# Kernel tuning notes

Hardware: AMD Instinct MI355X
Metric: run time of the kernel (lower is better)

## Reference

```python
import jax, jax.numpy as jnp
import numpy as np

EPS = 1e-6
N_HEADS, N_KV = 16, 4


def rmsnorm(x, w):
    return x * jax.lax.rsqrt(jnp.mean(x * x, axis=-1, keepdims=True) + EPS) * w


def setup_inputs() -> dict:
    key = jax.random.key(0)
    ks = jax.random.split(key, 9)
    B, T, D, F = 2, 2048, 2048, 8192
    KVD = N_KV * (D // N_HEADS)
    s = lambda k, shape, fan: (jax.random.normal(k, shape, jnp.float32) * (fan ** -0.5))
    return {
        "x": jax.random.normal(ks[0], (B, T, D), jnp.float32),
        "norm1_w": jnp.ones((D,), jnp.float32),
        "norm2_w": jnp.ones((D,), jnp.float32),
        "Wq": s(ks[1], (D, D), D),
        "Wk": s(ks[2], (D, KVD), D),
        "Wv": s(ks[3], (D, KVD), D),
        "Wo": s(ks[4], (D, D), D),
        "Wc": s(ks[5], (D, D), D),
        "W1": s(ks[6], (D, F), D),
        "W2": s(ks[7], (F, D), F),
        "W3": s(ks[8], (D, F), D),
    }


def reference(x, norm1_w, norm2_w, Wq, Wk, Wv, Wo, Wc, W1, W2, W3):
    B, T, D = x.shape
    dh = D // N_HEADS          # 128
    G = N_HEADS // N_KV        # groups per kv head
    scale = dh ** -0.5

    xn = rmsnorm(x, norm1_w)
    q = xn @ Wq                               # [B,T,D]
    pos = q @ Wc                              # CoPE stand-in: contextual positional bias on Q
    q = (q + pos).reshape(B, T, N_KV, G, dh)  # group q heads under their kv head
    k = (xn @ Wk).reshape(B, T, N_KV, dh)
    v = (xn @ Wv).reshape(B, T, N_KV, dh)

    # GQA without repeat_interleave: contract each group against shared K/V
    scores = jnp.einsum('bqkgd,bskd->bkgqs', q, k) * scale   # [B,KV,G,T,T]
    i = jnp.arange(T)
    causal = i[:, None] >= i[None, :]
    scores = jnp.where(causal, scores, -jnp.inf)
    w = jax.nn.softmax(scores, axis=-1)
    att = jnp.einsum('bkgqs,bskd->bqkgd', w, v).reshape(B, T, D)

    x = x + att @ Wo
    xn2 = rmsnorm(x, norm2_w)
    x = x + (jax.nn.silu(xn2 @ W1) * (xn2 @ W3)) @ W2
    return x
```

## Files before the change

### kernel.cpp

```cpp
#include <hip/hip_runtime.h>
#include <hip/hip_bf16.h>

typedef __attribute__((ext_vector_type(8))) short short8;
typedef __attribute__((ext_vector_type(4))) float floatx4;
typedef unsigned short ushort_t;

__device__ inline float b2f(ushort_t s) {
    return __uint_as_float(((unsigned int)s) << 16);
}
__device__ inline ushort_t f2b(float f) {
    unsigned int u = __float_as_uint(f);
    unsigned int r = 0x7fff + ((u >> 16) & 1);
    return (ushort_t)((u + r) >> 16);
}
__device__ inline unsigned int cvtpk(float lo, float hi) {
    unsigned int r;
    asm("v_cvt_pk_bf16_f32 %0, %1, %2" : "=v"(r) : "v"(lo), "v"(hi));
    return r;
}
__device__ inline void load8(const float* p, float* f) {
    float4 a = *(const float4*)p;
    float4 b = *(const float4*)(p + 4);
    f[0] = a.x; f[1] = a.y; f[2] = a.z; f[3] = a.w;
    f[4] = b.x; f[5] = b.y; f[6] = b.z; f[7] = b.w;
}
__device__ inline void gload16(const ushort_t* g, ushort_t* l) {
    __builtin_amdgcn_global_load_lds(
        (const __attribute__((address_space(1))) unsigned int*)g,
        (__attribute__((address_space(3))) unsigned int*)l, 16, 0, 0);
}
__device__ inline void lbar() {
    asm volatile("s_waitcnt lgkmcnt(0)" ::: "memory");
    __builtin_amdgcn_s_barrier();
    asm volatile("" ::: "memory");
}

__global__ __launch_bounds__(256) void transpose_all(
    const float* __restrict__ s0, const float* __restrict__ s1,
    const float* __restrict__ s2, const float* __restrict__ s3,
    const float* __restrict__ s4, const float* __restrict__ s5,
    const float* __restrict__ s6, const float* __restrict__ s7,
    ushort_t* d0, ushort_t* d1, ushort_t* d2, ushort_t* d3,
    ushort_t* d4, ushort_t* d5, ushort_t* d6, ushort_t* d7) {
    int id = blockIdx.x;
    const float* src; ushort_t* dst; int K, N;
    if (id < 1024)       { src = s0; dst = d0; K = 2048; N = 2048; }
    else if (id < 1280)  { id -= 1024;  src = s1; dst = d1; K = 2048; N = 512; }
    else if (id < 1536)  { id -= 1280;  src = s2; dst = d2; K = 2048; N = 512; }
    else if (id < 2560)  { id -= 1536;  src = s3; dst = d3; K = 2048; N = 2048; }
    else if (id < 3584)  { id -= 2560;  src = s4; dst = d4; K = 2048; N = 2048; }
    else if (id < 7680)  { id -= 3584;  src = s5; dst = d5; K = 2048; N = 8192; }
    else if (id < 11776) { id -= 7680;  src = s6; dst = d6; K = 2048; N = 8192; }
    else                 { id -= 11776; src = s7; dst = d7; K = 8192; N = 2048; }
    int tn = N >> 6;
    int kb = (id / tn) * 64, nb = (id % tn) * 64;
    __shared__ ushort_t tile[64][65];
    int t = threadIdx.x;
#pragma unroll
    for (int i = 0; i < 4; ++i) {
        int r = (t >> 4) + i * 16;
        int c = (t & 15) * 4;
        float4 v = *(const float4*)(src + (size_t)(kb + r) * N + nb + c);
        tile[c + 0][r] = f2b(v.x);
        tile[c + 1][r] = f2b(v.y);
        tile[c + 2][r] = f2b(v.z);
        tile[c + 3][r] = f2b(v.w);
    }
    __syncthreads();
#pragma unroll
    for (int i = 0; i < 2; ++i) {
        int s = t + i * 256;
        int n = s >> 3, kc = (s & 7) * 8;
        ushort_t o[8];
#pragma unroll
        for (int j = 0; j < 8; ++j) o[j] = tile[n][kc + j];
        *(uint4*)(dst + (size_t)(nb + n) * K + kb + kc) = *(const uint4*)o;
    }
}

__global__ __launch_bounds__(256) void rmsnorm_kernel(const float* __restrict__ x,
                                                      const float* __restrict__ w,
                                                      ushort_t* __restrict__ out, int D) {
    int row = blockIdx.x;
    int t = threadIdx.x;
    const float* xr = x + (size_t)row * D;
    float f[8];
    load8(xr + t * 8, f);
    float ss = 0.f;
#pragma unroll
    for (int i = 0; i < 8; ++i) ss += f[i] * f[i];
#pragma unroll
    for (int m = 1; m < 64; m <<= 1) ss += __shfl_xor(ss, m);
    __shared__ float wsum[4];
    if ((t & 63) == 0) wsum[t >> 6] = ss;
    __syncthreads();
    float tot = wsum[0] + wsum[1] + wsum[2] + wsum[3];
    float r = rsqrtf(tot / (float)D + 1e-6f);
    float wf[8];
    load8(w + t * 8, wf);
    ushort_t o[8];
#pragma unroll
    for (int i = 0; i < 8; ++i) o[i] = f2b(f[i] * r * wf[i]);
    *(uint4*)(out + (size_t)row * D + t * 8) = *(const uint4*)o;
}

__global__ __launch_bounds__(256) void reduce_out(const ushort_t* __restrict__ p,
                                                  const float* __restrict__ resid,
                                                  float* __restrict__ out, int n) {
    int stride = gridDim.x * 256;
    for (int i = blockIdx.x * 256 + threadIdx.x; i * 8 < n; i += stride) {
        int i8 = i * 8;
        uint4 a = *(const uint4*)(p + i8);
        uint4 b = *(const uint4*)(p + n + i8);
        const ushort_t* ae = (const ushort_t*)&a;
        const ushort_t* be = (const ushort_t*)&b;
        float rr[8];
        load8(resid + i8, rr);
        float o[8];
#pragma unroll
        for (int j = 0; j < 8; ++j) o[j] = b2f(ae[j]) + b2f(be[j]) + rr[j];
        *(float4*)(out + i8) = make_float4(o[0], o[1], o[2], o[3]);
        *(float4*)(out + i8 + 4) = make_float4(o[4], o[5], o[6], o[7]);
    }
}

__device__ inline void vm6() { asm volatile("s_waitcnt vmcnt(6)" ::: "memory"); }
__device__ inline void vm4() { asm volatile("s_waitcnt vmcnt(4)" ::: "memory"); }

template <int MODE>
__global__ __launch_bounds__(512, 2) void gemm8(const ushort_t* __restrict__ A,
                                                const ushort_t* __restrict__ Bt,
                                                const ushort_t* __restrict__ aux,
                                                const float* __restrict__ aux2,
                                                void* __restrict__ Cv,
                                                void* __restrict__ C2v,
                                                void* __restrict__ C3v,
                                                int M, int N, int Ksub, int lda) {
    __shared__ __align__(16) ushort_t Lds[2 * 32768];
    const int tid = threadIdx.x;
    const int wv = tid >> 6, lane = tid & 63;
    const int l16 = lane & 15, l4 = lane >> 4;
    const int wr = wv >> 2, wc = wv & 3;
    int nwg = gridDim.x;
    int per = nwg >> 3;
    int wg = (blockIdx.x & 7) * per + (blockIdx.x >> 3);
    int mtiles = M >> 8;
    int bx = wg & (mtiles - 1);
    int by = wg / mtiles;
    int bm = bx << 8, bn = by << 8;
    int koff = blockIdx.y * Ksub;

    const int sr = tid >> 3;
    const int scol = (((tid & 7) ^ (sr & 7)) << 3);
    const ushort_t* gA = A + (size_t)(bm + sr) * lda + scol + koff;
    const ushort_t* gB = Bt + (size_t)(bn + sr) * lda + scol + koff;
    ushort_t* ldsw = Lds + wv * 512;

    const int ktiles = Ksub >> 6;
    const int niter = ktiles >> 1;
    const int km = ktiles - 1;

#define STG_A(slot, j, kt) gload16(gA + (size_t)((j) * 64) * lda + ((kt) << 6), ldsw + (slot) * 32768 + (j) * 4096)
#define STG_B(slot, j, kt) gload16(gB + (size_t)((j) * 64) * lda + ((kt) << 6), ldsw + (slot) * 32768 + 16384 + (j) * 4096)

    STG_A(0, 0, 0); STG_A(0, 2, 0); STG_A(0, 1, 0); STG_A(0, 3, 0);
    STG_B(0, 0, 0); STG_B(0, 1, 0); STG_B(0, 2, 0); STG_B(0, 3, 0);
    STG_A(1, 0, 1); STG_A(1, 2, 1);
    STG_B(1, 0, 1); STG_B(1, 1, 1); STG_B(1, 2, 1); STG_B(1, 3, 1);
    vm6();
    asm volatile("" ::: "memory");
    __builtin_amdgcn_s_barrier();

    const int lx = l4 ^ (l16 & 7);
    floatx4 acc[8][4] = {};
    short8 aR[4][2], bR[4][2];

#define DSA(slot, mh) { _Pragma("unroll") for (int m = 0; m < 4; ++m) { \
    _Pragma("unroll") for (int kk = 0; kk < 2; ++kk) \
      aR[m][kk] = *(const short8*)(Lds + (slot) * 32768 + \
          (wr * 128 + (mh) * 64 + m * 16 + l16) * 64 + ((lx ^ (kk << 2)) << 3)); } }
#define DSB(slot, nh) { _Pragma("unroll") for (int n = 0; n < 2; ++n) { \
    _Pragma("unroll") for (int kk = 0; kk < 2; ++kk) \
      bR[(nh) * 2 + n][kk] = *(const short8*)(Lds + (slot) * 32768 + 16384 + \
          (wc * 64 + ((nh) * 2 + n) * 16 + l16) * 64 + ((lx ^ (kk << 2)) << 3)); } }
#define QUAD(mh, nlo) { _Pragma("unroll") for (int m = 0; m < 4; ++m) \
    _Pragma("unroll") for (int n = 0; n < 2; ++n) \
    _Pragma("unroll") for (int kk = 0; kk < 2; ++kk) \
      acc[(mh) * 4 + m][(nlo) + n] = __builtin_amdgcn_mfma_f32_16x16x32_bf16( \
          aR[m][kk], bR[(nlo) + n][kk], acc[(mh) * 4 + m][(nlo) + n], 0, 0, 0); }
#define PHASE(DS, ST, MH, NLO, VM) { \
    DS; ST; \
    asm volatile("" ::: "memory"); \
    __builtin_amdgcn_s_barrier(); \
    asm volatile("s_waitcnt lgkmcnt(0)" ::: "memory"); \
    __builtin_amdgcn_sched_barrier(0); \
    __builtin_amdgcn_s_setprio(1); \
    QUAD(MH, NLO); \
    __builtin_amdgcn_s_setprio(0); \
    VM; \
    asm volatile("" ::: "memory"); \
    __builtin_amdgcn_s_barrier(); }

    for (int it = 0; it < niter; ++it) {
        int t1 = 2 * it + 1;
        int t2 = (2 * it + 2) & km;
        int t3 = (2 * it + 3) & km;
        PHASE({ DSA(0, 0); DSB(0, 0); }, { STG_A(1, 1, t1); STG_A(1, 3, t1); }, 0, 0, );
        PHASE({ DSB(0, 1); },            { STG_A(0, 0, t2); STG_A(0, 2, t2); }, 0, 2, );
        PHASE({ DSA(0, 1); },            { STG_B(0, 0, t2); STG_B(0, 1, t2); }, 1, 2, );
        PHASE({ },                       { STG_B(0, 2, t2); STG_B(0, 3, t2); }, 1, 0, vm6(); );
        PHASE({ DSA(1, 0); DSB(1, 0); }, { STG_A(0, 1, t2); STG_A(0, 3, t2); }, 0, 0, );
        PHASE({ DSB(1, 1); },            { STG_A(1, 0, t3); STG_A(1, 2, t3); }, 0, 2, );
        PHASE({ DSA(1, 1); },            { STG_B(1, 0, t3); STG_B(1, 1, t3); }, 1, 2, );
        PHASE({ },                       { STG_B(1, 2, t3); STG_B(1, 3, t3); }, 1, 0, vm6(); );
    }

#pragma unroll
    for (int mi = 0; mi < 8; ++mi)
#pragma unroll
        for (int ni = 0; ni < 4; ++ni)
#pragma unroll
            for (int r = 0; r < 4; ++r) {
                int row = bm + wr * 128 + mi * 16 + l4 * 4 + r;
                int col = bn + wc * 64 + ni * 16 + l16;
                size_t idx = (size_t)row * N + col;
                float v = acc[mi][ni][r];
                if (MODE == 0) {
                    ((ushort_t*)Cv)[idx] = f2b(v);
                } else if (MODE == 1) {
                    ((ushort_t*)Cv)[idx] = f2b(v + b2f(aux[idx]));
                } else if (MODE == 2) {
                    float h = b2f(aux[idx]);
                    ((ushort_t*)Cv)[idx] = f2b((h / (1.f + __expf(-h))) * v);
                } else if (MODE == 3) {
                    ((ushort_t*)Cv)[(size_t)blockIdx.y * M * N + idx] = f2b(v);
                } else if (MODE == 5) {
                    ((float*)Cv)[idx] = v + aux2[idx];
                } else if (MODE == 6) {
                    if (bn < 2048) {
                        ((ushort_t*)Cv)[(size_t)row * 2048 + col] = f2b(v);
                    } else if (bn < 2560) {
                        ((ushort_t*)C2v)[(size_t)row * 512 + (col - 2048)] = f2b(v);
                    } else {
                        ((ushort_t*)C3v)[(size_t)(col - 2560) * 4096 + row] = f2b(v);
                    }
                }
            }
#undef STG_A
#undef STG_B
#undef DSA
#undef DSB
#undef QUAD
#undef PHASE
}

template <int MODE>
__global__ __launch_bounds__(512, 1) void gemm8h(const ushort_t* __restrict__ A,
                                                 const ushort_t* __restrict__ Bt,
                                                 const ushort_t* __restrict__ aux,
                                                 const float* __restrict__ aux2,
                                                 void* __restrict__ Cv,
                                                 int M, int N, int K) {
    __shared__ __align__(16) ushort_t Lds[2 * 24576];
    const int tid = threadIdx.x;
    const int wv = tid >> 6, lane = tid & 63;
    const int l16 = lane & 15, l4 = lane >> 4;
    const int wr = wv >> 2, wc = wv & 3;
    int nwg = gridDim.x;
    int per = nwg >> 3;
    int wg = (blockIdx.x & 7) * per + (blockIdx.x >> 3);
    int mtiles = M >> 7;
    int bx = wg & (mtiles - 1);
    int by = wg / mtiles;
    int bm = bx << 7, bn = by << 8;

    const int sr = tid >> 3;
    const int scol = (((tid & 7) ^ (sr & 7)) << 3);
    const ushort_t* gA = A + (size_t)(bm + sr) * K + scol;
    const ushort_t* gB = Bt + (size_t)(bn + sr) * K + scol;
    ushort_t* ldsw = Lds + wv * 512;

    const int ktiles = K >> 6;
    const int niter = ktiles >> 1;
    const int km = ktiles - 1;

#define HSTG_A(slot, j, kt) gload16(gA + (size_t)((j) * 64) * K + ((kt) << 6), ldsw + (slot) * 24576 + (j) * 4096)
#define HSTG_B(slot, j, kt) gload16(gB + (size_t)((j) * 64) * K + ((kt) << 6), ldsw + (slot) * 24576 + 8192 + (j) * 4096)

    HSTG_A(0, 0, 0); HSTG_A(0, 1, 0);
    HSTG_B(0, 0, 0); HSTG_B(0, 1, 0); HSTG_B(0, 2, 0); HSTG_B(0, 3, 0);
    HSTG_A(1, 0, 1); HSTG_A(1, 1, 1);
    HSTG_B(1, 0, 1); HSTG_B(1, 1, 1);
    vm4();
    asm volatile("" ::: "memory");
    __builtin_amdgcn_s_barrier();

    const int lx = l4 ^ (l16 & 7);
    floatx4 acc[4][4] = {};
    short8 aR[2][2], bR[4][2];

#define HDSA(slot, mh) { _Pragma("unroll") for (int m = 0; m < 2; ++m) { \
    _Pragma("unroll") for (int kk = 0; kk < 2; ++kk) \
      aR[m][kk] = *(const short8*)(Lds + (slot) * 24576 + \
          (wr * 64 + (mh) * 32 + m * 16 + l16) * 64 + ((lx ^ (kk << 2)) << 3)); } }
#define HDSB(slot, nh) { _Pragma("unroll") for (int n = 0; n < 2; ++n) { \
    _Pragma("unroll") for (int kk = 0; kk < 2; ++kk) \
      bR[(nh) * 2 + n][kk] = *(const short8*)(Lds + (slot) * 24576 + 8192 + \
          (wc * 64 + ((nh) * 2 + n) * 16 + l16) * 64 + ((lx ^ (kk << 2)) << 3)); } }
#define HQUAD(mh, nlo) { _Pragma("unroll") for (int m = 0; m < 2; ++m) \
    _Pragma("unroll") for (int n = 0; n < 2; ++n) \
    _Pragma("unroll") for (int kk = 0; kk < 2; ++kk) \
      acc[(mh) * 2 + m][(nlo) + n] = __builtin_amdgcn_mfma_f32_16x16x32_bf16( \
          aR[m][kk], bR[(nlo) + n][kk], acc[(mh) * 2 + m][(nlo) + n], 0, 0, 0); }
#define HPHASE(DS, ST, MH, NLO, VM) { \
    DS; ST; \
    asm volatile("" ::: "memory"); \
    __builtin_amdgcn_s_barrier(); \
    asm volatile("s_waitcnt lgkmcnt(0)" ::: "memory"); \
    __builtin_amdgcn_sched_barrier(0); \
    __builtin_amdgcn_s_setprio(1); \
    HQUAD(MH, NLO); \
    __builtin_amdgcn_s_setprio(0); \
    VM; \
    asm volatile("" ::: "memory"); \
    __builtin_amdgcn_s_barrier(); }

    for (int it = 0; it < niter; ++it) {
        int t1 = 2 * it + 1;
        int t2 = (2 * it + 2) & km;
        int t3 = (2 * it + 3) & km;
        HPHASE({ HDSA(0, 0); HDSB(0, 0); }, { HSTG_B(1, 2, t1); HSTG_B(1, 3, t1); }, 0, 0, );
        HPHASE({ HDSB(0, 1); },             { },                                     0, 2, );
        HPHASE({ HDSA(0, 1); },             { HSTG_B(0, 0, t2); HSTG_B(0, 1, t2); }, 1, 2, );
        HPHASE({ },                         { HSTG_B(0, 2, t2); HSTG_B(0, 3, t2); }, 1, 0, vm4(); );
        HPHASE({ HDSA(1, 0); HDSB(1, 0); }, { HSTG_A(0, 0, t2); HSTG_A(0, 1, t2); }, 0, 0, );
        HPHASE({ HDSB(1, 1); },             { },                                     0, 2, );
        HPHASE({ HDSA(1, 1); },             { HSTG_B(1, 0, t3); HSTG_B(1, 1, t3); }, 1, 2, );
        HPHASE({ },                         { HSTG_A(1, 0, t3); HSTG_A(1, 1, t3); }, 1, 0, vm4(); );
    }

#pragma unroll
    for (int mi = 0; mi < 4; ++mi)
#pragma unroll
        for (int ni = 0; ni < 4; ++ni)
#pragma unroll
            for (int r = 0; r < 4; ++r) {
                int row = bm + wr * 64 + mi * 16 + l4 * 4 + r;
                int col = bn + wc * 64 + ni * 16 + l16;
                size_t idx = (size_t)row * N + col;
                float v = acc[mi][ni][r];
                if (MODE == 1) ((ushort_t*)Cv)[idx] = f2b(v + b2f(aux[idx]));
                else if (MODE == 5) ((float*)Cv)[idx] = v + aux2[idx];
            }
#undef HSTG_A
#undef HSTG_B
#undef HDSA
#undef HDSB
#undef HQUAD
#undef HPHASE
}

#define QB 64
#define SB 64

__global__ __launch_bounds__(256, 2) void attn_kernel(const ushort_t* __restrict__ Q,
                                                      const ushort_t* __restrict__ Kb,
                                                      const ushort_t* __restrict__ VbT,
                                                      ushort_t* __restrict__ O, int Tlen) {
    const int D = 2048, KVD = 512, dh = 128;
    const int MTOK = 4096;
    int p = blockIdx.x, h = blockIdx.y, b = blockIdx.z;
    int kv = h >> 2;
    int t = threadIdx.x, wave = t >> 6, lane = t & 63;
    int l16 = lane & 15, l4 = lane >> 4;
    __shared__ __align__(16) ushort_t Ks[2][SB][dh + 8];
    __shared__ __align__(16) ushort_t Vt[2][dh][SB + 8];
    __shared__ __align__(16) unsigned int Ps2[4][16][36];
    const float scale = 0.08838834764831845f;
    const ushort_t* Kg = Kb + ((size_t)(b * Tlen) + (t >> 4)) * KVD + kv * dh + (t & 15) * 8;
    const ushort_t* Vg = VbT + (size_t)(kv * dh + (t >> 3)) * MTOK + b * Tlen + (t & 7) * 8;

    for (int side = 0; side < 2; ++side) {
        int qt = side ? p : (31 - p);
        int qbase = qt * QB;
        int qfrag = qbase + wave * 16;
        int qcol = qfrag + l16;
        short8 qf[4];
        const ushort_t* Qrow = Q + ((size_t)(b * Tlen) + qfrag + l16) * D + h * dh;
#pragma unroll
        for (int kk = 0; kk < 4; ++kk) qf[kk] = *(const short8*)(Qrow + kk * 32 + l4 * 8);
        floatx4 o_acc[8] = {};
        float m_s = -INFINITY, l_s = 0.f;
        int nst = qt + 1;
        uint4 kreg[4], vreg[4];
#pragma unroll
        for (int p4 = 0; p4 < 4; ++p4) {
            kreg[p4] = *(const uint4*)(Kg + (size_t)(p4 * 16) * KVD);
            vreg[p4] = *(const uint4*)(Vg + (size_t)(p4 * 32) * MTOK);
        }
        lbar();
#pragma unroll
        for (int p4 = 0; p4 < 4; ++p4) {
            *(uint4*)(&Ks[0][(t >> 4) + p4 * 16][(t & 15) * 8]) = kreg[p4];
            *(uint4*)(&Vt[0][(t >> 3) + p4 * 32][(t & 7) * 8]) = vreg[p4];
        }
        if (nst > 1) {
#pragma unroll
            for (int p4 = 0; p4 < 4; ++p4) {
                kreg[p4] = *(const uint4*)(Kg + (size_t)(SB + p4 * 16) * KVD);
                vreg[p4] = *(const uint4*)(Vg + (size_t)(p4 * 32) * MTOK + SB);
            }
        }
        lbar();
        for (int st = 0; st < nst; ++st) {
            int cur = st & 1;
            int s0 = st * SB;
            if (st + 1 < nst) {
#pragma unroll
                for (int p4 = 0; p4 < 4; ++p4) {
                    *(uint4*)(&Ks[cur ^ 1][(t >> 4) + p4 * 16][(t & 15) * 8]) = kreg[p4];
                    *(uint4*)(&Vt[cur ^ 1][(t >> 3) + p4 * 32][(t & 7) * 8]) = vreg[p4];
                }
            }
            if (st + 2 < nst) {
                size_t off = (size_t)(st + 2) * SB;
#pragma unroll
                for (int p4 = 0; p4 < 4; ++p4) {
                    kreg[p4] = *(const uint4*)(Kg + (off + p4 * 16) * KVD);
                    vreg[p4] = *(const uint4*)(Vg + (size_t)(p4 * 32) * MTOK + off);
                }
            }
            floatx4 sa[4] = {};
            __builtin_amdgcn_s_setprio(1);
#pragma unroll
            for (int ss = 0; ss < 4; ++ss)
#pragma unroll
                for (int kk = 0; kk < 4; ++kk) {
                    short8 kf = *(const short8*)(&Ks[cur][ss * 16 + l16][kk * 32 + l4 * 8]);
                    sa[ss] = __builtin_amdgcn_mfma_f32_16x16x32_bf16(kf, qf[kk], sa[ss], 0, 0, 0);
                }
            __builtin_amdgcn_s_setprio(0);
            float sv[4][4];
            float pmax = -INFINITY;
#pragma unroll
            for (int ss = 0; ss < 4; ++ss)
#pragma unroll
                for (int r = 0; r < 4; ++r) {
                    int krow = s0 + ss * 16 + l4 * 4 + r;
                    float v = sa[ss][r] * scale;
                    if (krow > qcol) v = -INFINITY;
                    sv[ss][r] = v;
                    pmax = fmaxf(pmax, v);
                }
            pmax = fmaxf(pmax, __shfl_xor(pmax, 16));
            pmax = fmaxf(pmax, __shfl_xor(pmax, 32));
            bool skip = __all(pmax <= m_s + 8.f);
            float mn = skip ? m_s : fmaxf(m_s, pmax);
            float rsum = 0.f;
#pragma unroll
            for (int ss = 0; ss < 4; ++ss)
#pragma unroll
                for (int r = 0; r < 4; ++r) {
                    float pv = __expf(sv[ss][r] - mn);
                    sv[ss][r] = pv;
                    rsum += pv;
                }
            rsum += __shfl_xor(rsum, 16);
            rsum += __shfl_xor(rsum, 32);
            if (skip) {
                l_s += rsum;
            } else {
                float esc = __expf(m_s - mn);
                l_s = l_s * esc + rsum;
                m_s = mn;
                float ef[4];
#pragma unroll
                for (int r = 0; r < 4; ++r) ef[r] = __shfl(esc, l4 * 4 + r);
#pragma unroll
                for (int c = 0; c < 8; ++c)
#pragma unroll
                    for (int r = 0; r < 4; ++r) o_acc[c][r] *= ef[r];
            }
#pragma unroll
            for (int ss = 0; ss < 4; ++ss) {
                uint2 pk;
                pk.x = cvtpk(sv[ss][0], sv[ss][1]);
                pk.y = cvtpk(sv[ss][2], sv[ss][3]);
                *(uint2*)&Ps2[wave][l16][ss * 8 + l4 * 2] = pk;
            }
            short8 pa[2];
#pragma unroll
            for (int kk = 0; kk < 2; ++kk) {
                uint4 pv4 = *(const uint4*)&Ps2[wave][l16][kk * 16 + l4 * 4];
                pa[kk] = *(const short8*)&pv4;
            }
            __builtin_amdgcn_s_setprio(1);
#pragma unroll
            for (int c = 0; c < 8; ++c)
#pragma unroll
                for (int kk = 0; kk < 2; ++kk) {
                    short8 vf = *(const short8*)(&Vt[cur][c * 16 + l16][kk * 32 + l4 * 8]);
                    o_acc[c] = __builtin_amdgcn_mfma_f32_16x16x32_bf16(pa[kk], vf, o_acc[c], 0, 0, 0);
                }
            __builtin_amdgcn_s_setprio(0);
            lbar();
        }
        float linv[4];
#pragma unroll
        for (int r = 0; r < 4; ++r) linv[r] = 1.f / __shfl(l_s, l4 * 4 + r);
        ushort_t* Osh = &Ks[0][0][0];
#pragma unroll
        for (int c = 0; c < 8; ++c)
#pragma unroll
            for (int r = 0; r < 4; ++r)
                Osh[(wave * 16 + l4 * 4 + r) * 136 + c * 16 + l16] = f2b(o_acc[c][r] * linv[r]);
        lbar();
        {
            int orow = t >> 2, occ = (t & 3) * 32;
            const ushort_t* srcp = Osh + orow * 136 + occ;
            ushort_t* dstp = O + ((size_t)(b * Tlen) + qbase + orow) * D + h * dh + occ;
#pragma unroll
            for (int k = 0; k < 4; ++k)
                *(uint4*)(dstp + k * 8) = *(const uint4*)(srcp + k * 8);
        }
    }
}

extern "C" void kernel_launch(void* const* d_in, const int* in_sizes, int n_in,
                              void* d_out, int out_size, void* d_ws, size_t ws_size,
                              hipStream_t stream) {
    const float* x   = (const float*)d_in[0];
    const float* n1w = (const float*)d_in[1];
    const float* n2w = (const float*)d_in[2];
    const float* Wq  = (const float*)d_in[3];
    const float* Wk  = (const float*)d_in[4];
    const float* Wv  = (const float*)d_in[5];
    const float* Wo  = (const float*)d_in[6];
    const float* Wc  = (const float*)d_in[7];
    const float* W1  = (const float*)d_in[8];
    const float* W2  = (const float*)d_in[9];
    const float* W3  = (const float*)d_in[10];
    float* out = (float*)d_out;

    const int B = 2, T = 2048, D = 2048, F = 8192, KVD = 512;
    const int M = B * T;
    const size_t XD   = (size_t)M * D * 2;
    const size_t XDF  = (size_t)M * D * 4;
    const size_t KVSZ = (size_t)M * KVD * 2;
    const size_t MF   = (size_t)M * F * 2;
    const size_t WDD  = (size_t)D * D * 2;
    const size_t WQKV = (size_t)(D + 2 * KVD) * D * 2;
    const size_t WDF  = (size_t)D * F * 2;

    char* w = (char*)d_ws;
    ushort_t* xn    = (ushort_t*)(w);
    ushort_t* qtmp  = (ushort_t*)(w + XD);
    ushort_t* qfin  = (ushort_t*)(w + 2 * XD);
    float*    x2f   = (float*)   (w + 3 * XD);
    ushort_t* kbuf  = (ushort_t*)(w + 3 * XD + XDF);
    ushort_t* vbufT = (ushort_t*)(w + 3 * XD + XDF + KVSZ);
    ushort_t* h1    = (ushort_t*)(w + 3 * XD + XDF + 2 * KVSZ);
    char* wt = w + 3 * XD + XDF + 2 * KVSZ + MF;
    ushort_t* WqkvT = (ushort_t*)(wt);
    ushort_t* WcT   = (ushort_t*)(wt + WQKV);
    ushort_t* WoT   = (ushort_t*)(wt + WQKV + WDD);
    ushort_t* W1T   = (ushort_t*)(wt + WQKV + 2 * WDD);
    ushort_t* W3T   = (ushort_t*)(wt + WQKV + 2 * WDD + WDF);
    ushort_t* W2T   = (ushort_t*)(wt + WQKV + 2 * WDD + 2 * WDF);

    dim3 blk(256);
    dim3 blk8(512);

    transpose_all<<<15872, blk, 0, stream>>>(
        Wq, Wk, Wv, Wc, Wo, W1, W3, W2,
        WqkvT, WqkvT + (size_t)2048 * D, WqkvT + (size_t)2560 * D,
        WcT, WoT, W1T, W3T, W2T);

    rmsnorm_kernel<<<M, blk, 0, stream>>>(x, n1w, xn, D);
    gemm8<6><<<dim3((M / 256) * (3072 / 256)), blk8, 0, stream>>>(
        xn, WqkvT, nullptr, nullptr, qtmp, kbuf, vbufT, M, 3072, D, D);
    gemm8h<1><<<dim3((M / 128) * (D / 256)), blk8, 0, stream>>>(
        qtmp, WcT, qtmp, nullptr, qfin, M, D, D);
    attn_kernel<<<dim3(16, 16, B), blk, 0, stream>>>(qfin, kbuf, vbufT, qtmp, T);
    gemm8h<5><<<dim3((M / 128) * (D / 256)), blk8, 0, stream>>>(
        qtmp, WoT, nullptr, x, x2f, M, D, D);
    rmsnorm_kernel<<<M, blk, 0, stream>>>(x2f, n2w, xn, D);
    gemm8<0><<<dim3((M / 256) * (F / 256)), blk8, 0, stream>>>(
        xn, W1T, nullptr, nullptr, h1, nullptr, nullptr, M, F, D, D);
    gemm8<2><<<dim3((M / 256) * (F / 256)), blk8, 0, stream>>>(
        xn, W3T, h1, nullptr, h1, nullptr, nullptr, M, F, D, D);
    gemm8<3><<<dim3((M / 256) * (D / 256), 2), blk8, 0, stream>>>(
        h1, W2T, nullptr, nullptr, xn, nullptr, nullptr, M, D, F / 2, F);
    reduce_out<<<1024, blk, 0, stream>>>(xn, x2f, out, M * D);
}
```

Before: 791.6 us.

## Enlarge attention query tile to 128 rows with two fragments per wave

Each wave of the attention kernel now processes two 16-row query fragments (query block 128 instead of 64), so every K/V tile staged in shared memory feeds twice as many MFMAs. This halves K/V global loads and LDS staging per query and amortizes barriers. In exchange the grid halves to 256 blocks, occupancy drops to one block per CU via launch bounds, register pressure roughly doubles for accumulators, and causal masking wastes more work on the diagonal tile.

```diff
diff --git a/kernel.cpp b/kernel.cpp
--- a/kernel.cpp
+++ b/kernel.cpp
@@ -360,10 +360,10 @@
 #undef HPHASE
 }
 
-#define QB 64
+#define QB 128
 #define SB 64
 
-__global__ __launch_bounds__(256, 2) void attn_kernel(const ushort_t* __restrict__ Q,
+__global__ __launch_bounds__(256, 1) void attn_kernel(const ushort_t* __restrict__ Q,
                                                       const ushort_t* __restrict__ Kb,
                                                       const ushort_t* __restrict__ VbT,
                                                       ushort_t* __restrict__ O, int Tlen) {
@@ -375,23 +375,27 @@
     int l16 = lane & 15, l4 = lane >> 4;
     __shared__ __align__(16) ushort_t Ks[2][SB][dh + 8];
     __shared__ __align__(16) ushort_t Vt[2][dh][SB + 8];
-    __shared__ __align__(16) unsigned int Ps2[4][16][36];
+    __shared__ __align__(16) unsigned int Ps2[8][16][36];
     const float scale = 0.08838834764831845f;
     const ushort_t* Kg = Kb + ((size_t)(b * Tlen) + (t >> 4)) * KVD + kv * dh + (t & 15) * 8;
     const ushort_t* Vg = VbT + (size_t)(kv * dh + (t >> 3)) * MTOK + b * Tlen + (t & 7) * 8;
 
     for (int side = 0; side < 2; ++side) {
-        int qt = side ? p : (31 - p);
+        int qt = side ? p : (15 - p);
         int qbase = qt * QB;
-        int qfrag = qbase + wave * 16;
-        int qcol = qfrag + l16;
-        short8 qf[4];
-        const ushort_t* Qrow = Q + ((size_t)(b * Tlen) + qfrag + l16) * D + h * dh;
-#pragma unroll
-        for (int kk = 0; kk < 4; ++kk) qf[kk] = *(const short8*)(Qrow + kk * 32 + l4 * 8);
-        floatx4 o_acc[8] = {};
-        float m_s = -INFINITY, l_s = 0.f;
-        int nst = qt + 1;
+        int qw = qbase + wave * 32;
+        short8 qf[2][4];
+#pragma unroll
+        for (int f = 0; f < 2; ++f) {
+            const ushort_t* Qrow = Q + ((size_t)(b * Tlen) + qw + f * 16 + l16) * D + h * dh;
+#pragma unroll
+            for (int kk = 0; kk < 4; ++kk) qf[f][kk] = *(const short8*)(Qrow + kk * 32 + l4 * 8);
+        }
+        floatx4 o_acc[2][8] = {};
+        float m_s[2], l_s[2];
+#pragma unroll
+        for (int f = 0; f < 2; ++f) { m_s[f] = -INFINITY; l_s[f] = 0.f; }
+        int nst = 2 * qt + 2;
         uint4 kreg[4], vreg[4];
 #pragma unroll
         for (int p4 = 0; p4 < 4; ++p4) {
@@ -430,69 +434,74 @@
                     vreg[p4] = *(const uint4*)(Vg + (size_t)(p4 * 32) * MTOK + off);
                 }
             }
-            floatx4 sa[4] = {};
+            floatx4 sa[2][4] = {};
             __builtin_amdgcn_s_setprio(1);
 #pragma unroll
             for (int ss = 0; ss < 4; ++ss)
 #pragma unroll
                 for (int kk = 0; kk < 4; ++kk) {
                     short8 kf = *(const short8*)(&Ks[cur][ss * 16 + l16][kk * 32 + l4 * 8]);
-                    sa[ss] = __builtin_amdgcn_mfma_f32_16x16x32_bf16(kf, qf[kk], sa[ss], 0, 0, 0);
+                    sa[0][ss] = __builtin_amdgcn_mfma_f32_16x16x32_bf16(kf, qf[0][kk], sa[0][ss], 0, 0, 0);
+                    sa[1][ss] = __builtin_amdgcn_mfma_f32_16x16x32_bf16(kf, qf[1][kk], sa[1][ss], 0, 0, 0);
                 }
             __builtin_amdgcn_s_setprio(0);
-            float sv[4][4];
-            float pmax = -INFINITY;
-#pragma unroll
-            for (int ss = 0; ss < 4; ++ss)
-#pragma unroll
-                for (int r = 0; r < 4; ++r) {
-                    int krow = s0 + ss * 16 + l4 * 4 + r;
-                    float v = sa[ss][r] * scale;
-                    if (krow > qcol) v = -INFINITY;
-                    sv[ss][r] = v;
-                    pmax = fmaxf(pmax, v);
-                }
-            pmax = fmaxf(pmax, __shfl_xor(pmax, 16));
-            pmax = fmaxf(pmax, __shfl_xor(pmax, 32));
-            bool skip = __all(pmax <= m_s + 8.f);
-            float mn = skip ? m_s : fmaxf(m_s, pmax);
-            float rsum = 0.f;
-#pragma unroll
-            for (int ss = 0; ss < 4; ++ss)
-#pragma unroll
-                for (int r = 0; r < 4; ++r) {
-                    float pv = __expf(sv[ss][r] - mn);
-                    sv[ss][r] = pv;
-                    rsum += pv;
-                }
-            rsum += __shfl_xor(rsum, 16);
-            rsum += __shfl_xor(rsum, 32);
-            if (skip) {
-                l_s += rsum;
-            } else {
-                float esc = __expf(m_s - mn);
-                l_s = l_s * esc + rsum;
-                m_s = mn;
-                float ef[4];
-#pragma unroll
-                for (int r = 0; r < 4; ++r) ef[r] = __shfl(esc, l4 * 4 + r);
-#pragma unroll
-                for (int c = 0; c < 8; ++c)
-#pragma unroll
-                    for (int r = 0; r < 4; ++r) o_acc[c][r] *= ef[r];
-            }
-#pragma unroll
-            for (int ss = 0; ss < 4; ++ss) {
-                uint2 pk;
-                pk.x = cvtpk(sv[ss][0], sv[ss][1]);
-                pk.y = cvtpk(sv[ss][2], sv[ss][3]);
-                *(uint2*)&Ps2[wave][l16][ss * 8 + l4 * 2] = pk;
-            }
-            short8 pa[2];
-#pragma unroll
-            for (int kk = 0; kk < 2; ++kk) {
-                uint4 pv4 = *(const uint4*)&Ps2[wave][l16][kk * 16 + l4 * 4];
-                pa[kk] = *(const short8*)&pv4;
+            short8 pa[2][2];
+#pragma unroll
+            for (int f = 0; f < 2; ++f) {
+                int qcol = qw + f * 16 + l16;
+                float sv[4][4];
+                float pmax = -INFINITY;
+#pragma unroll
+                for (int ss = 0; ss < 4; ++ss)
+#pragma unroll
+                    for (int r = 0; r < 4; ++r) {
+                        int krow = s0 + ss * 16 + l4 * 4 + r;
+                        float v = sa[f][ss][r] * scale;
+                        if (krow > qcol) v = -INFINITY;
+                        sv[ss][r] = v;
+                        pmax = fmaxf(pmax, v);
+                    }
+                pmax = fmaxf(pmax, __shfl_xor(pmax, 16));
+                pmax = fmaxf(pmax, __shfl_xor(pmax, 32));
+                bool skip = __all(pmax <= m_s[f] + 8.f);
+                float mn = skip ? m_s[f] : fmaxf(m_s[f], pmax);
+                float rsum = 0.f;
+#pragma unroll
+                for (int ss = 0; ss < 4; ++ss)
+#pragma unroll
+                    for (int r = 0; r < 4; ++r) {
+                        float pv = __expf(sv[ss][r] - mn);
+                        sv[ss][r] = pv;
+                        rsum += pv;
+                    }
+                rsum += __shfl_xor(rsum, 16);
+                rsum += __shfl_xor(rsum, 32);
+                if (skip) {
+                    l_s[f] += rsum;
+                } else {
+                    float esc = __expf(m_s[f] - mn);
+                    l_s[f] = l_s[f] * esc + rsum;
+                    m_s[f] = mn;
+                    float ef[4];
+#pragma unroll
+                    for (int r = 0; r < 4; ++r) ef[r] = __shfl(esc, l4 * 4 + r);
+#pragma unroll
+                    for (int c = 0; c < 8; ++c)
+#pragma unroll
+                        for (int r = 0; r < 4; ++r) o_acc[f][c][r] *= ef[r];
+                }
+#pragma unroll
+                for (int ss = 0; ss < 4; ++ss) {
+                    uint2 pk;
+                    pk.x = cvtpk(sv[ss][0], sv[ss][1]);
+                    pk.y = cvtpk(sv[ss][2], sv[ss][3]);
+                    *(uint2*)&Ps2[wave * 2 + f][l16][ss * 8 + l4 * 2] = pk;
+                }
+#pragma unroll
+                for (int kk = 0; kk < 2; ++kk) {
+                    uint4 pv4 = *(const uint4*)&Ps2[wave * 2 + f][l16][kk * 16 + l4 * 4];
+                    pa[f][kk] = *(const short8*)&pv4;
+                }
             }
             __builtin_amdgcn_s_setprio(1);
 #pragma unroll
@@ -500,27 +509,32 @@
 #pragma unroll
                 for (int kk = 0; kk < 2; ++kk) {
                     short8 vf = *(const short8*)(&Vt[cur][c * 16 + l16][kk * 32 + l4 * 8]);
-                    o_acc[c] = __builtin_amdgcn_mfma_f32_16x16x32_bf16(pa[kk], vf, o_acc[c], 0, 0, 0);
+                    o_acc[0][c] = __builtin_amdgcn_mfma_f32_16x16x32_bf16(pa[0][kk], vf, o_acc[0][c], 0, 0, 0);
+                    o_acc[1][c] = __builtin_amdgcn_mfma_f32_16x16x32_bf16(pa[1][kk], vf, o_acc[1][c], 0, 0, 0);
                 }
             __builtin_amdgcn_s_setprio(0);
             lbar();
         }
-        float linv[4];
-#pragma unroll
-        for (int r = 0; r < 4; ++r) linv[r] = 1.f / __shfl(l_s, l4 * 4 + r);
         ushort_t* Osh = &Ks[0][0][0];
 #pragma unroll
-        for (int c = 0; c < 8; ++c)
-#pragma unroll
-            for (int r = 0; r < 4; ++r)
-                Osh[(wave * 16 + l4 * 4 + r) * 136 + c * 16 + l16] = f2b(o_acc[c][r] * linv[r]);
+        for (int f = 0; f < 2; ++f) {
+            float linv[4];
+#pragma unroll
+            for (int r = 0; r < 4; ++r) linv[r] = 1.f / __shfl(l_s[f], l4 * 4 + r);
+#pragma unroll
+            for (int c = 0; c < 8; ++c)
+#pragma unroll
+                for (int r = 0; r < 4; ++r)
+                    Osh[(wave * 32 + f * 16 + l4 * 4 + r) * 136 + c * 16 + l16] =
+                        f2b(o_acc[f][c][r] * linv[r]);
+        }
         lbar();
         {
-            int orow = t >> 2, occ = (t & 3) * 32;
+            int orow = t >> 1, occ = (t & 1) * 64;
             const ushort_t* srcp = Osh + orow * 136 + occ;
             ushort_t* dstp = O + ((size_t)(b * Tlen) + qbase + orow) * D + h * dh + occ;
 #pragma unroll
-            for (int k = 0; k < 4; ++k)
+            for (int k = 0; k < 8; ++k)
                 *(uint4*)(dstp + k * 8) = *(const uint4*)(srcp + k * 8);
         }
     }
@@ -581,7 +595,7 @@
         xn, WqkvT, nullptr, nullptr, qtmp, kbuf, vbufT, M, 3072, D, D);
     gemm8h<1><<<dim3((M / 128) * (D / 256)), blk8, 0, stream>>>(
         qtmp, WcT, qtmp, nullptr, qfin, M, D, D);
-    attn_kernel<<<dim3(16, 16, B), blk, 0, stream>>>(qfin, kbuf, vbufT, qtmp, T);
+    attn_kernel<<<dim3(8, 16, B), blk, 0, stream>>>(qfin, kbuf, vbufT, qtmp, T);
     gemm8h<5><<<dim3((M / 128) * (D / 256)), blk8, 0, stream>>>(
         qtmp, WoT, nullptr, x, x2f, M, D, D);
     rmsnorm_kernel<<<M, blk, 0, stream>>>(x2f, n2w, xn, D);
```

New measurement: 777.5 us. No clear change (-1.8%).
